# Kernel optimization log

Hardware: AMD Instinct MI355X
Metric: run time of the kernel (lower is better)

The kernel has to match this reference:

```python
import jax, jax.numpy as jnp
import numpy as np


def _pos_enc(seq_len, d_model, dtype):
    # PositionalEncoding2D buffer: interleaved sin/cos, standard transformer PE
    pos = jnp.arange(seq_len, dtype=dtype)[:, None]                      # [S,1]
    div = jnp.exp(jnp.arange(0, d_model, 2, dtype=dtype) * (-(np.log(10000.0) / d_model)))  # [d/2]
    pe = jnp.zeros((seq_len, d_model), dtype=dtype)
    pe = pe.at[:, 0::2].set(jnp.sin(pos * div))
    pe = pe.at[:, 1::2].set(jnp.cos(pos * div))
    return pe


def setup_inputs() -> dict:
    key = jax.random.key(0)
    k1, k2 = jax.random.split(key)
    B, C, H, W = 32, 384, 32, 32
    d = C
    x = jax.random.normal(k1, (B, C, H, W), dtype=jnp.float32)
    # fused QKV projection weight (stored as [d, 3d] so y = x @ W + b)
    Wqkv = jax.random.normal(k2, (d, 3 * d), dtype=jnp.float32) * (1.0 / np.sqrt(d))
    b = jnp.zeros((3 * d,), dtype=jnp.float32)
    return {"x": x, "W": Wqkv, "b": b}


def reference(x, W, b):
    B, C, H, Wd = x.shape
    d = C
    S = H * Wd
    xs = x.reshape(B, C, S).transpose(0, 2, 1)          # [B,S,d]
    xs = xs + _pos_enc(S, d, xs.dtype)                  # add positional encoding
    qkv = xs @ W + b                                    # [B,S,3d]
    q, k, v = jnp.split(qkv, 3, axis=-1)                # each [B,S,d]
    scores = jnp.einsum('bqd,bkd->bqk', q, k) / (d ** 0.5)  # [B,S,S]
    attn = jax.nn.softmax(scores, axis=-1)
    weighted = jnp.einsum('bqk,bkd->bqd', attn, v)      # [B,S,d]
    return weighted.transpose(0, 2, 1).reshape(B, C, H, Wd)
```

## Files before the change

kernel.cpp:

```cpp
#include <hip/hip_runtime.h>
#include <hip/hip_bf16.h>
#include <math.h>

typedef __attribute__((ext_vector_type(8))) __bf16 bf16x8;
typedef __attribute__((ext_vector_type(4))) float f32x4;

#define S_LEN 1024
#define D_MODEL 384
#define BATCH 32
#define N3 1152
#define KVB 32
#define NT (S_LEN / KVB)

#define MFMA16(a, b, c) __builtin_amdgcn_mfma_f32_16x16x32_bf16((a), (b), (c), 0, 0, 0)

static __device__ __forceinline__ ushort f2bf(float f) {
    __bf16 h = (__bf16)f;
    return __builtin_bit_cast(ushort, h);
}
static __device__ __forceinline__ uint pk2(float a, float b) {
    return (uint)f2bf(a) | ((uint)f2bf(b) << 16);
}

__global__ void pe_kernel(float* peT) {
    int idx = blockIdx.x * 256 + threadIdx.x;
    int k = idx >> 10, s = idx & 1023;
    float e = -(float)((k >> 1) * 2) * (logf(10000.0f) / (float)D_MODEL);
    float div = expf(e);
    float a = (float)s * div;
    peT[idx] = (k & 1) ? cosf(a) : sinf(a);
}

__global__ void wt_kernel(const float* __restrict__ W, ushort* __restrict__ Wt) {
    __shared__ float tile[32][33];
    int n0 = blockIdx.x * 32, k0 = blockIdx.y * 32;
    int tx = threadIdx.x, ty = threadIdx.y;
#pragma unroll
    for (int r = 0; r < 4; ++r) {
        int kl = ty * 4 + r;
        tile[kl][tx] = W[(size_t)(k0 + kl) * N3 + n0 + tx];
    }
    __syncthreads();
#pragma unroll
    for (int r = 0; r < 4; ++r) {
        int nl = ty * 4 + r;
        Wt[(size_t)(n0 + nl) * D_MODEL + k0 + tx] = f2bf(tile[tx][nl]);
    }
}

__global__ void astage_kernel(const float* __restrict__ x, const float* __restrict__ peT,
                              ushort* __restrict__ A) {
    __shared__ float tile[32][33];
    int s0 = blockIdx.x * 32, k0 = blockIdx.y * 32, b = blockIdx.z;
    int tx = threadIdx.x, ty = threadIdx.y;
#pragma unroll
    for (int r = 0; r < 4; ++r) {
        int kl = ty * 4 + r;
        tile[kl][tx] = x[(size_t)(b * D_MODEL + k0 + kl) * S_LEN + s0 + tx]
                     + peT[(size_t)(k0 + kl) * S_LEN + s0 + tx];
    }
    __syncthreads();
#pragma unroll
    for (int r = 0; r < 4; ++r) {
        int sl = ty * 4 + r;
        A[(size_t)(b * S_LEN + s0 + sl) * D_MODEL + k0 + tx] = f2bf(tile[tx][sl]);
    }
}

__global__ __launch_bounds__(256) void qkv_gemm(const ushort* __restrict__ A,
                                                const ushort* __restrict__ Wt,
                                                const float* __restrict__ bias,
                                                ushort* __restrict__ Qb,
                                                ushort* __restrict__ Ktl,
                                                ushort* __restrict__ Vtl) {
    __shared__ __align__(16) ushort As[128 * 32];
    __shared__ __align__(16) ushort Bs[128 * 32];
    int id = blockIdx.x;
    int g = id / 288, loc = id % 288;
    int nt_ = loc / 32, mt_ = g * 32 + (loc % 32);
    int m0 = mt_ * 128, n0 = nt_ * 128;
    int tid = threadIdx.x;
    int wave = tid >> 6, lane = tid & 63;
    int i16 = lane & 15, gq = lane >> 4;
    int wr = wave >> 1, wc = wave & 1;
    f32x4 acc[4][4] = {};
    for (int ks = 0; ks < 12; ++ks) {
        int k0 = ks * 32;
        __syncthreads();
#pragma unroll
        for (int i = 0; i < 2; ++i) {
            int off = (wave * 2 + i) * 1024;
            int row = (off >> 6) + (lane >> 2);
            int kc = lane & 3;
            const ushort* ga = A + (size_t)(m0 + row) * D_MODEL + k0 + kc * 8;
            __builtin_amdgcn_global_load_lds(
                (const __attribute__((address_space(1))) uint32_t*)ga,
                (__attribute__((address_space(3))) uint32_t*)((char*)As + off), 16, 0, 0);
            const ushort* gb = Wt + (size_t)(n0 + row) * D_MODEL + k0 + kc * 8;
            __builtin_amdgcn_global_load_lds(
                (const __attribute__((address_space(1))) uint32_t*)gb,
                (__attribute__((address_space(3))) uint32_t*)((char*)Bs + off), 16, 0, 0);
        }
        __syncthreads();
        bf16x8 af[4], bfr[4];
#pragma unroll
        for (int mt = 0; mt < 4; ++mt) {
            int row = wr * 64 + mt * 16 + i16;
            af[mt] = *reinterpret_cast<const bf16x8*>(&As[row * 32 + gq * 8]);
        }
#pragma unroll
        for (int nt = 0; nt < 4; ++nt) {
            int row = wc * 64 + nt * 16 + i16;
            bfr[nt] = *reinterpret_cast<const bf16x8*>(&Bs[row * 32 + gq * 8]);
        }
#pragma unroll
        for (int mt = 0; mt < 4; ++mt)
#pragma unroll
            for (int nt = 0; nt < 4; ++nt)
                acc[mt][nt] = MFMA16(af[mt], bfr[nt], acc[mt][nt]);
    }
    if (n0 < D_MODEL) {
#pragma unroll
        for (int nt = 0; nt < 4; ++nt) {
            int n = n0 + wc * 64 + nt * 16 + i16;
            float bv = bias[n];
#pragma unroll
            for (int mt = 0; mt < 4; ++mt)
#pragma unroll
                for (int r = 0; r < 4; ++r) {
                    int m = m0 + wr * 64 + mt * 16 + gq * 4 + r;
                    Qb[(size_t)m * D_MODEL + n] = f2bf(acc[mt][nt][r] + bv);
                }
        }
    } else if (n0 < 2 * D_MODEL) {
        int b = m0 >> 10;
#pragma unroll
        for (int nt = 0; nt < 4; ++nt) {
            int n = n0 + wc * 64 + nt * 16 + i16;
            float bv = bias[n];
            int k2 = n - D_MODEL;
            int slotx = k2 >> 3, within = k2 & 7;
#pragma unroll
            for (int mt = 0; mt < 4; ++mt)
#pragma unroll
                for (int r = 0; r < 4; ++r) {
                    int m = m0 + wr * 64 + mt * 16 + gq * 4 + r;
                    int s = m & 1023;
                    int t = s >> 5, j = s & 31;
                    size_t idx = (size_t)(b * 32 + t) * 12288 + j * 384
                               + (((slotx ^ (j & 7)) << 3) + within);
                    Ktl[idx] = f2bf(acc[mt][nt][r] + bv);
                }
        }
    } else {
        int b = m0 >> 10;
#pragma unroll
        for (int nt = 0; nt < 4; ++nt) {
            int n = n0 + wc * 64 + nt * 16 + i16;
            float bv = bias[n];
            int c = n - 2 * D_MODEL;
            int cx = (c >> 1) & 3;
#pragma unroll
            for (int mt = 0; mt < 4; ++mt) {
                int m = m0 + wr * 64 + mt * 16 + gq * 4;
                int s = m & 1023;
                int t = s >> 5, j = s & 31;
                size_t idx = (size_t)(b * 32 + t) * 12288 + c * 32
                           + ((((j >> 3) ^ cx) << 3) + (j & 7));
                ushort4 p4;
                p4.x = f2bf(acc[mt][nt][0] + bv);
                p4.y = f2bf(acc[mt][nt][1] + bv);
                p4.z = f2bf(acc[mt][nt][2] + bv);
                p4.w = f2bf(acc[mt][nt][3] + bv);
                *reinterpret_cast<ushort4*>(&Vtl[idx]) = p4;
            }
        }
    }
}

__global__ __launch_bounds__(256, 2) void attn_kernel(const ushort* __restrict__ Qb,
                                                      const ushort* __restrict__ Ktl,
                                                      const ushort* __restrict__ Vtl,
                                                      float* __restrict__ out) {
    __shared__ __align__(16) ushort Ks[32 * 384];
    __shared__ __align__(16) ushort Vts[2][384 * 32];
    __shared__ __align__(16) ushort Pq[2][4 * 32 * 8];
    __shared__ float Ltab[2][2][2][16];
    int id = blockIdx.x;
    int xcd = id & 7, slot = (id >> 3) & 3, qt = id >> 5;
    int b = slot * 8 + xcd;
    int tid = threadIdx.x;
    int wave = tid >> 6, lane = tid & 63;
    int i16 = lane & 15, gq = lane >> 4;
    int qg = wave & 1, h = wave >> 1;
    int q0w = qt * 64 + qg * 32;

    auto stage_K = [&](int tt) {
        const ushort* pan = Ktl + (size_t)(b * 32 + tt) * 12288;
#pragma unroll
        for (int r = 0; r < 6; ++r) {
            int ii = wave * 6 + r;
            const ushort* ga = pan + ii * 512 + lane * 8;
            __builtin_amdgcn_global_load_lds(
                (const __attribute__((address_space(1))) uint32_t*)ga,
                (__attribute__((address_space(3))) uint32_t*)((char*)Ks + ii * 1024), 16, 0, 0);
        }
    };
    auto stage_V = [&](int tt, int bi) {
        const ushort* pan = Vtl + (size_t)(b * 32 + tt) * 12288;
#pragma unroll
        for (int r = 0; r < 6; ++r) {
            int ii = wave * 6 + r;
            const ushort* ga = pan + ii * 512 + lane * 8;
            __builtin_amdgcn_global_load_lds(
                (const __attribute__((address_space(1))) uint32_t*)ga,
                (__attribute__((address_space(3))) uint32_t*)((char*)&Vts[bi][0] + ii * 1024), 16, 0, 0);
        }
    };

    stage_K(0);
    stage_V(0, 0);

    bf16x8 qf[12][2];
    const ushort* Qb0 = Qb + (size_t)(b * S_LEN + q0w + i16) * D_MODEL;
    const ushort* Qb1 = Qb + (size_t)(b * S_LEN + q0w + 16 + i16) * D_MODEL;
#pragma unroll
    for (int kt = 0; kt < 12; ++kt) {
        qf[kt][0] = *reinterpret_cast<const bf16x8*>(Qb0 + kt * 32 + gq * 8);
        qf[kt][1] = *reinterpret_cast<const bf16x8*>(Qb1 + kt * 32 + gq * 8);
    }

    f32x4 oc[12][2] = {};
    float lsum0 = 0.f, lsum1 = 0.f;
    const float sl2e = 0.05103103630798287f * 1.4426950408889634f;

    char* PqB = (char*)&Pq[qg][0];
    const int krow = (h * 16 + i16) * 768;
    const int ksw  = (i16 & 7) << 4;
    const int kgq  = gq * 16;
    const int vx   = (gq * 16) ^ (((i16 >> 1) & 3) << 4);

    for (int t = 0; t < NT; ++t) {
        asm volatile("s_waitcnt vmcnt(6) lgkmcnt(0)" ::: "memory");
        __builtin_amdgcn_s_barrier();
        __builtin_amdgcn_sched_barrier(0);

        const char* Kb = (const char*)Ks;
        f32x4 sacc0 = {}, sacc1 = {};
        __builtin_amdgcn_s_setprio(1);
#pragma unroll
        for (int kt = 0; kt < 12; ++kt) {
            bf16x8 kf = *reinterpret_cast<const bf16x8*>(
                Kb + krow + (((kt * 64) | kgq) ^ ksw));
            sacc0 = MFMA16(kf, qf[kt][0], sacc0);
            sacc1 = MFMA16(kf, qf[kt][1], sacc1);
        }
        __builtin_amdgcn_s_setprio(0);

        float p00 = exp2f(sacc0[0] * sl2e), p01 = exp2f(sacc0[1] * sl2e);
        float p02 = exp2f(sacc0[2] * sl2e), p03 = exp2f(sacc0[3] * sl2e);
        float p10 = exp2f(sacc1[0] * sl2e), p11 = exp2f(sacc1[1] * sl2e);
        float p12 = exp2f(sacc1[2] * sl2e), p13 = exp2f(sacc1[3] * sl2e);
        lsum0 += (p00 + p01) + (p02 + p03);
        lsum1 += (p10 + p11) + (p12 + p13);
        {
            int pw = (h * 2 + (gq >> 1)) * 512 + (gq & 1) * 8;
            uint2 w0; w0.x = pk2(p00, p01); w0.y = pk2(p02, p03);
            uint2 w1; w1.x = pk2(p10, p11); w1.y = pk2(p12, p13);
            *reinterpret_cast<uint2*>(PqB + pw + i16 * 16) = w0;
            *reinterpret_cast<uint2*>(PqB + pw + (16 + i16) * 16) = w1;
        }
        asm volatile("s_waitcnt vmcnt(0) lgkmcnt(0)" ::: "memory");
        __builtin_amdgcn_s_barrier();
        __builtin_amdgcn_sched_barrier(0);
        if (t + 1 < NT) {
            stage_K(t + 1);
            stage_V(t + 1, (t + 1) & 1);
        }

        bf16x8 pf0 = *reinterpret_cast<const bf16x8*>(PqB + gq * 512 + i16 * 16);
        bf16x8 pf1 = *reinterpret_cast<const bf16x8*>(PqB + gq * 512 + (16 + i16) * 16);
        const char* Vb = (const char*)&Vts[t & 1][0];
        __builtin_amdgcn_s_setprio(1);
#pragma unroll
        for (int ct = 0; ct < 12; ++ct) {
            bf16x8 vf = *reinterpret_cast<const bf16x8*>(
                Vb + (h * 12 + ct) * 1024 + i16 * 64 + vx);
            oc[ct][0] = MFMA16(vf, pf0, oc[ct][0]);
            oc[ct][1] = MFMA16(vf, pf1, oc[ct][1]);
        }
        __builtin_amdgcn_s_setprio(0);
    }

    lsum0 += __shfl_xor(lsum0, 16); lsum0 += __shfl_xor(lsum0, 32);
    lsum1 += __shfl_xor(lsum1, 16); lsum1 += __shfl_xor(lsum1, 32);
    __syncthreads();
    if (gq == 0) {
        Ltab[qg][h][0][i16] = lsum0;
        Ltab[qg][h][1][i16] = lsum1;
    }
    __syncthreads();
    float inv0 = 1.0f / (Ltab[qg][0][0][i16] + Ltab[qg][1][0][i16]);
    float inv1 = 1.0f / (Ltab[qg][0][1][i16] + Ltab[qg][1][1][i16]);

    float* obase = out + (size_t)b * D_MODEL * S_LEN + q0w + i16;
#pragma unroll
    for (int ct = 0; ct < 12; ++ct)
#pragma unroll
        for (int r = 0; r < 4; ++r) {
            int c = h * 192 + ct * 16 + gq * 4 + r;
            obase[(size_t)c * S_LEN] = oc[ct][0][r] * inv0;
            obase[(size_t)c * S_LEN + 16] = oc[ct][1][r] * inv1;
        }
}

extern "C" void kernel_launch(void* const* d_in, const int* in_sizes, int n_in,
                              void* d_out, int out_size, void* d_ws, size_t ws_size,
                              hipStream_t stream) {
    const float* x    = (const float*)d_in[0];
    const float* W    = (const float*)d_in[1];
    const float* bias = (const float*)d_in[2];
    float* out = (float*)d_out;

    char* ws = (char*)d_ws;
    ushort* A_bf = (ushort*)(ws);
    ushort* Wt   = (ushort*)(ws + 25165824);
    float*  peT  = (float*)(ws + 26050560);
    ushort* Qb   = (ushort*)(ws + 27623424);
    ushort* Ktl  = (ushort*)(ws + 52789248);
    ushort* Vtl  = (ushort*)(ws + 77955072);

    pe_kernel<<<1536, 256, 0, stream>>>(peT);
    wt_kernel<<<dim3(36, 12), dim3(32, 8), 0, stream>>>(W, Wt);
    astage_kernel<<<dim3(32, 12, 32), dim3(32, 8), 0, stream>>>(x, peT, A_bf);
    qkv_gemm<<<2304, 256, 0, stream>>>(A_bf, Wt, bias, Qb, Ktl, Vtl);
    attn_kernel<<<512, 256, 0, stream>>>(Qb, Ktl, Vtl, out);
}
```

Measured before the change: 155.0 us.

## Widen attention KV tile to 64 with 8 waves splitting keys and shuffled P

Doubles the key/value block per iteration to 64 and moves to 512-thread blocks where 4 query groups of 16 rows and 2 key halves share the staged K/V tiles, with a final cross-wave reduction of partial outputs through LDS. The P matrix is redistributed via lane shuffles instead of an LDS round trip, and exp and bf16 packing use raw v_exp_f32 and v_cvt_pk_bf16_f32 instructions. The QKV GEMM epilogue is changed to write the new 64-row swizzled K/V layout. The aim is fewer barriers per key and less LDS traffic, but LDS use grows to about 148 KB per block, which may limit occupancy. The wait now drains all loads before each iteration, which removes the previous overlap of prefetch with compute.

After: 161.1 us. +4.0%, slower.

```diff
diff --git a/kernel.cpp b/kernel.cpp
--- a/kernel.cpp
+++ b/kernel.cpp
@@ -9,7 +9,7 @@
 #define D_MODEL 384
 #define BATCH 32
 #define N3 1152
-#define KVB 32
+#define KVB 64
 #define NT (S_LEN / KVB)
 
 #define MFMA16(a, b, c) __builtin_amdgcn_mfma_f32_16x16x32_bf16((a), (b), (c), 0, 0, 0)
@@ -18,8 +18,11 @@
     __bf16 h = (__bf16)f;
     return __builtin_bit_cast(ushort, h);
 }
-static __device__ __forceinline__ uint pk2(float a, float b) {
-    return (uint)f2bf(a) | ((uint)f2bf(b) << 16);
+static __device__ __forceinline__ float exp2a(float x) {
+    float r; asm("v_exp_f32 %0, %1" : "=v"(r) : "v"(x)); return r;
+}
+static __device__ __forceinline__ uint cvtpk(float a, float b) {
+    uint r; asm("v_cvt_pk_bf16_f32 %0, %1, %2" : "=v"(r) : "v"(a), "v"(b)); return r;
 }
 
 __global__ void pe_kernel(float* peT) {
@@ -139,16 +142,16 @@
             int n = n0 + wc * 64 + nt * 16 + i16;
             float bv = bias[n];
             int k2 = n - D_MODEL;
-            int slotx = k2 >> 3, within = k2 & 7;
+            int slotk = k2 >> 3, within = k2 & 7;
 #pragma unroll
             for (int mt = 0; mt < 4; ++mt)
 #pragma unroll
                 for (int r = 0; r < 4; ++r) {
                     int m = m0 + wr * 64 + mt * 16 + gq * 4 + r;
                     int s = m & 1023;
-                    int t = s >> 5, j = s & 31;
-                    size_t idx = (size_t)(b * 32 + t) * 12288 + j * 384
-                               + (((slotx ^ (j & 7)) << 3) + within);
+                    int t = s >> 6, j = s & 63;
+                    size_t idx = (size_t)(b * 16 + t) * 24576 + j * 384
+                               + (((slotk ^ (j & 7)) << 3) + within);
                     Ktl[idx] = f2bf(acc[mt][nt][r] + bv);
                 }
         }
@@ -159,13 +162,13 @@
             int n = n0 + wc * 64 + nt * 16 + i16;
             float bv = bias[n];
             int c = n - 2 * D_MODEL;
-            int cx = (c >> 1) & 3;
+            int cx = c & 7;
 #pragma unroll
             for (int mt = 0; mt < 4; ++mt) {
                 int m = m0 + wr * 64 + mt * 16 + gq * 4;
                 int s = m & 1023;
-                int t = s >> 5, j = s & 31;
-                size_t idx = (size_t)(b * 32 + t) * 12288 + c * 32
+                int t = s >> 6, j = s & 63;
+                size_t idx = (size_t)(b * 16 + t) * 24576 + c * 64
                            + ((((j >> 3) ^ cx) << 3) + (j & 7));
                 ushort4 p4;
                 p4.x = f2bf(acc[mt][nt][0] + bv);
@@ -178,99 +181,101 @@
     }
 }
 
-__global__ __launch_bounds__(256, 2) void attn_kernel(const ushort* __restrict__ Qb,
+__global__ __launch_bounds__(512, 2) void attn_kernel(const ushort* __restrict__ Qb,
                                                       const ushort* __restrict__ Ktl,
                                                       const ushort* __restrict__ Vtl,
                                                       float* __restrict__ out) {
-    __shared__ __align__(16) ushort Ks[32 * 384];
-    __shared__ __align__(16) ushort Vts[2][384 * 32];
-    __shared__ __align__(16) ushort Pq[2][4 * 32 * 8];
-    __shared__ float Ltab[2][2][2][16];
+    __shared__ __align__(16) char smem[49152 * 3 + 512];
     int id = blockIdx.x;
     int xcd = id & 7, slot = (id >> 3) & 3, qt = id >> 5;
     int b = slot * 8 + xcd;
     int tid = threadIdx.x;
     int wave = tid >> 6, lane = tid & 63;
     int i16 = lane & 15, gq = lane >> 4;
-    int qg = wave & 1, h = wave >> 1;
-    int q0w = qt * 64 + qg * 32;
+    int qg = wave & 3, h = wave >> 2;
+    int q0w = qt * 64 + qg * 16;
 
     auto stage_K = [&](int tt) {
-        const ushort* pan = Ktl + (size_t)(b * 32 + tt) * 12288;
+        const ushort* pan = Ktl + (size_t)(b * 16 + tt) * 24576;
 #pragma unroll
         for (int r = 0; r < 6; ++r) {
             int ii = wave * 6 + r;
             const ushort* ga = pan + ii * 512 + lane * 8;
             __builtin_amdgcn_global_load_lds(
                 (const __attribute__((address_space(1))) uint32_t*)ga,
-                (__attribute__((address_space(3))) uint32_t*)((char*)Ks + ii * 1024), 16, 0, 0);
+                (__attribute__((address_space(3))) uint32_t*)(smem + ii * 1024), 16, 0, 0);
         }
     };
     auto stage_V = [&](int tt, int bi) {
-        const ushort* pan = Vtl + (size_t)(b * 32 + tt) * 12288;
+        const ushort* pan = Vtl + (size_t)(b * 16 + tt) * 24576;
+        char* dst = smem + 49152 + bi * 49152;
 #pragma unroll
         for (int r = 0; r < 6; ++r) {
             int ii = wave * 6 + r;
             const ushort* ga = pan + ii * 512 + lane * 8;
             __builtin_amdgcn_global_load_lds(
                 (const __attribute__((address_space(1))) uint32_t*)ga,
-                (__attribute__((address_space(3))) uint32_t*)((char*)&Vts[bi][0] + ii * 1024), 16, 0, 0);
+                (__attribute__((address_space(3))) uint32_t*)(dst + ii * 1024), 16, 0, 0);
         }
     };
 
     stage_K(0);
     stage_V(0, 0);
 
-    bf16x8 qf[12][2];
-    const ushort* Qb0 = Qb + (size_t)(b * S_LEN + q0w + i16) * D_MODEL;
-    const ushort* Qb1 = Qb + (size_t)(b * S_LEN + q0w + 16 + i16) * D_MODEL;
-#pragma unroll
-    for (int kt = 0; kt < 12; ++kt) {
-        qf[kt][0] = *reinterpret_cast<const bf16x8*>(Qb0 + kt * 32 + gq * 8);
-        qf[kt][1] = *reinterpret_cast<const bf16x8*>(Qb1 + kt * 32 + gq * 8);
-    }
-
-    f32x4 oc[12][2] = {};
-    float lsum0 = 0.f, lsum1 = 0.f;
+    bf16x8 qf[12];
+    const ushort* Qr = Qb + (size_t)(b * S_LEN + q0w + i16) * D_MODEL;
+#pragma unroll
+    for (int kt = 0; kt < 12; ++kt)
+        qf[kt] = *reinterpret_cast<const bf16x8*>(Qr + kt * 32 + gq * 8);
+
+    f32x4 oc[24] = {};
+    float lsum = 0.f;
     const float sl2e = 0.05103103630798287f * 1.4426950408889634f;
-
-    char* PqB = (char*)&Pq[qg][0];
-    const int krow = (h * 16 + i16) * 768;
-    const int ksw  = (i16 & 7) << 4;
-    const int kgq  = gq * 16;
-    const int vx   = (gq * 16) ^ (((i16 >> 1) & 3) << 4);
+    const int sw = i16 & 7;
+    const int jb = h * 32;
+    const int srcA = ((gq & 1) << 5) + i16;
+    const int srcB = srcA + 16;
+    const int jhsel = gq >> 1;
 
     for (int t = 0; t < NT; ++t) {
-        asm volatile("s_waitcnt vmcnt(6) lgkmcnt(0)" ::: "memory");
+        asm volatile("s_waitcnt vmcnt(0) lgkmcnt(0)" ::: "memory");
         __builtin_amdgcn_s_barrier();
         __builtin_amdgcn_sched_barrier(0);
 
-        const char* Kb = (const char*)Ks;
+        const char* Kb = (const char*)smem;
         f32x4 sacc0 = {}, sacc1 = {};
         __builtin_amdgcn_s_setprio(1);
 #pragma unroll
         for (int kt = 0; kt < 12; ++kt) {
-            bf16x8 kf = *reinterpret_cast<const bf16x8*>(
-                Kb + krow + (((kt * 64) | kgq) ^ ksw));
-            sacc0 = MFMA16(kf, qf[kt][0], sacc0);
-            sacc1 = MFMA16(kf, qf[kt][1], sacc1);
+            const char* k0p = Kb + (jb + i16) * 768 + (((kt * 4 + gq) ^ sw) << 4);
+            const char* k1p = Kb + (jb + 16 + i16) * 768 + (((kt * 4 + gq) ^ sw) << 4);
+            bf16x8 kf0 = *reinterpret_cast<const bf16x8*>(k0p);
+            bf16x8 kf1 = *reinterpret_cast<const bf16x8*>(k1p);
+            sacc0 = MFMA16(kf0, qf[kt], sacc0);
+            sacc1 = MFMA16(kf1, qf[kt], sacc1);
         }
         __builtin_amdgcn_s_setprio(0);
 
-        float p00 = exp2f(sacc0[0] * sl2e), p01 = exp2f(sacc0[1] * sl2e);
-        float p02 = exp2f(sacc0[2] * sl2e), p03 = exp2f(sacc0[3] * sl2e);
-        float p10 = exp2f(sacc1[0] * sl2e), p11 = exp2f(sacc1[1] * sl2e);
-        float p12 = exp2f(sacc1[2] * sl2e), p13 = exp2f(sacc1[3] * sl2e);
-        lsum0 += (p00 + p01) + (p02 + p03);
-        lsum1 += (p10 + p11) + (p12 + p13);
-        {
-            int pw = (h * 2 + (gq >> 1)) * 512 + (gq & 1) * 8;
-            uint2 w0; w0.x = pk2(p00, p01); w0.y = pk2(p02, p03);
-            uint2 w1; w1.x = pk2(p10, p11); w1.y = pk2(p12, p13);
-            *reinterpret_cast<uint2*>(PqB + pw + i16 * 16) = w0;
-            *reinterpret_cast<uint2*>(PqB + pw + (16 + i16) * 16) = w1;
-        }
-        asm volatile("s_waitcnt vmcnt(0) lgkmcnt(0)" ::: "memory");
+        float p00 = exp2a(sacc0[0] * sl2e), p01 = exp2a(sacc0[1] * sl2e);
+        float p02 = exp2a(sacc0[2] * sl2e), p03 = exp2a(sacc0[3] * sl2e);
+        float p10 = exp2a(sacc1[0] * sl2e), p11 = exp2a(sacc1[1] * sl2e);
+        float p12 = exp2a(sacc1[2] * sl2e), p13 = exp2a(sacc1[3] * sl2e);
+        lsum += ((p00 + p01) + (p02 + p03)) + ((p10 + p11) + (p12 + p13));
+
+        uint u00 = cvtpk(p00, p01), u01 = cvtpk(p02, p03);
+        uint u10 = cvtpk(p10, p11), u11 = cvtpk(p12, p13);
+        uint tA0 = __shfl(u00, srcA, 64), tA1 = __shfl(u10, srcA, 64);
+        uint tA2 = __shfl(u01, srcA, 64), tA3 = __shfl(u11, srcA, 64);
+        uint tB0 = __shfl(u00, srcB, 64), tB1 = __shfl(u10, srcB, 64);
+        uint tB2 = __shfl(u01, srcB, 64), tB3 = __shfl(u11, srcB, 64);
+        uint4 wv;
+        wv.x = jhsel ? tA1 : tA0;
+        wv.y = jhsel ? tA3 : tA2;
+        wv.z = jhsel ? tB1 : tB0;
+        wv.w = jhsel ? tB3 : tB2;
+        bf16x8 pf = __builtin_bit_cast(bf16x8, wv);
+
+        asm volatile("s_waitcnt lgkmcnt(0)" ::: "memory");
         __builtin_amdgcn_s_barrier();
         __builtin_amdgcn_sched_barrier(0);
         if (t + 1 < NT) {
@@ -278,40 +283,44 @@
             stage_V(t + 1, (t + 1) & 1);
         }
 
-        bf16x8 pf0 = *reinterpret_cast<const bf16x8*>(PqB + gq * 512 + i16 * 16);
-        bf16x8 pf1 = *reinterpret_cast<const bf16x8*>(PqB + gq * 512 + (16 + i16) * 16);
-        const char* Vb = (const char*)&Vts[t & 1][0];
+        const char* Vb = smem + 49152 + (t & 1) * 49152;
         __builtin_amdgcn_s_setprio(1);
 #pragma unroll
-        for (int ct = 0; ct < 12; ++ct) {
-            bf16x8 vf = *reinterpret_cast<const bf16x8*>(
-                Vb + (h * 12 + ct) * 1024 + i16 * 64 + vx);
-            oc[ct][0] = MFMA16(vf, pf0, oc[ct][0]);
-            oc[ct][1] = MFMA16(vf, pf1, oc[ct][1]);
+        for (int ct = 0; ct < 24; ++ct) {
+            const char* vp = Vb + (ct * 16 + i16) * 128 + (((h * 4 + gq) ^ sw) << 4);
+            bf16x8 vf = *reinterpret_cast<const bf16x8*>(vp);
+            oc[ct] = MFMA16(vf, pf, oc[ct]);
         }
         __builtin_amdgcn_s_setprio(0);
     }
 
-    lsum0 += __shfl_xor(lsum0, 16); lsum0 += __shfl_xor(lsum0, 32);
-    lsum1 += __shfl_xor(lsum1, 16); lsum1 += __shfl_xor(lsum1, 32);
+    lsum += __shfl_xor(lsum, 16);
+    lsum += __shfl_xor(lsum, 32);
     __syncthreads();
-    if (gq == 0) {
-        Ltab[qg][h][0][i16] = lsum0;
-        Ltab[qg][h][1][i16] = lsum1;
+    float* Ored = (float*)smem;
+    float* Lred = (float*)(smem + 98304);
+    if (h == 0) {
+        float* Oq = Ored + qg * 6144;
+#pragma unroll
+        for (int ct = 0; ct < 24; ++ct)
+#pragma unroll
+            for (int r = 0; r < 4; ++r)
+                Oq[(ct * 16 + gq * 4 + r) * 16 + i16] = oc[ct][r];
+        if (gq == 0) Lred[qg * 16 + i16] = lsum;
     }
     __syncthreads();
-    float inv0 = 1.0f / (Ltab[qg][0][0][i16] + Ltab[qg][1][0][i16]);
-    float inv1 = 1.0f / (Ltab[qg][0][1][i16] + Ltab[qg][1][1][i16]);
-
-    float* obase = out + (size_t)b * D_MODEL * S_LEN + q0w + i16;
-#pragma unroll
-    for (int ct = 0; ct < 12; ++ct)
-#pragma unroll
-        for (int r = 0; r < 4; ++r) {
-            int c = h * 192 + ct * 16 + gq * 4 + r;
-            obase[(size_t)c * S_LEN] = oc[ct][0][r] * inv0;
-            obase[(size_t)c * S_LEN + 16] = oc[ct][1][r] * inv1;
-        }
+    if (h == 1) {
+        const float* Oq = Ored + qg * 6144;
+        float inv = 1.0f / (lsum + Lred[qg * 16 + i16]);
+        float* ob = out + (size_t)b * D_MODEL * S_LEN + q0w + i16;
+#pragma unroll
+        for (int ct = 0; ct < 24; ++ct)
+#pragma unroll
+            for (int r = 0; r < 4; ++r) {
+                int c = ct * 16 + gq * 4 + r;
+                ob[(size_t)c * S_LEN] = (oc[ct][r] + Oq[c * 16 + i16]) * inv;
+            }
+    }
 }
 
 extern "C" void kernel_launch(void* const* d_in, const int* in_sizes, int n_in,
@@ -334,5 +343,5 @@
     wt_kernel<<<dim3(36, 12), dim3(32, 8), 0, stream>>>(W, Wt);
     astage_kernel<<<dim3(32, 12, 32), dim3(32, 8), 0, stream>>>(x, peT, A_bf);
     qkv_gemm<<<2304, 256, 0, stream>>>(A_bf, Wt, bias, Qb, Ktl, Vtl);
-    attn_kernel<<<512, 256, 0, stream>>>(Qb, Ktl, Vtl, out);
-}
+    attn_kernel<<<512, 512, 0, stream>>>(Qb, Ktl, Vtl, out);
+}
```

## Warp-specialize attention into QK/softmax and PV waves with 128-query blocks

Applied to the files above, without the earlier changes.

Rewrites the attention kernel into a 512-thread block covering 128 queries. Four waves compute QK^T and exp and write P to double-buffered LDS, while four other waves run PV one tile behind, with K and V each double-buffered and software-pipelined. The goal is to overlap the softmax/QK phase with the PV MFMAs and to halve K/V re-staging per query. Exp and bf16 packing are swapped for raw v_exp_f32 and v_cvt_pk_bf16_f32 instructions. This raises LDS use and register pressure (48 accumulators per PV wave) and halves the grid to 256 blocks, which may leave some CUs idle.

Result: faster. 139.1 us (-10.3%).

```diff
diff --git a/kernel.cpp b/kernel.cpp
--- a/kernel.cpp
+++ b/kernel.cpp
@@ -18,8 +18,11 @@
     __bf16 h = (__bf16)f;
     return __builtin_bit_cast(ushort, h);
 }
-static __device__ __forceinline__ uint pk2(float a, float b) {
-    return (uint)f2bf(a) | ((uint)f2bf(b) << 16);
+static __device__ __forceinline__ float exp2a(float x) {
+    float r; asm("v_exp_f32 %0, %1" : "=v"(r) : "v"(x)); return r;
+}
+static __device__ __forceinline__ uint cvtpk(float a, float b) {
+    uint r; asm("v_cvt_pk_bf16_f32 %0, %1, %2" : "=v"(r) : "v"(a), "v"(b)); return r;
 }
 
 __global__ void pe_kernel(float* peT) {
@@ -139,7 +142,7 @@
             int n = n0 + wc * 64 + nt * 16 + i16;
             float bv = bias[n];
             int k2 = n - D_MODEL;
-            int slotx = k2 >> 3, within = k2 & 7;
+            int slotk = k2 >> 3, within = k2 & 7;
 #pragma unroll
             for (int mt = 0; mt < 4; ++mt)
 #pragma unroll
@@ -148,7 +151,7 @@
                     int s = m & 1023;
                     int t = s >> 5, j = s & 31;
                     size_t idx = (size_t)(b * 32 + t) * 12288 + j * 384
-                               + (((slotx ^ (j & 7)) << 3) + within);
+                               + (((slotk ^ (j & 7)) << 3) + within);
                     Ktl[idx] = f2bf(acc[mt][nt][r] + bv);
                 }
         }
@@ -178,140 +181,187 @@
     }
 }
 
-__global__ __launch_bounds__(256, 2) void attn_kernel(const ushort* __restrict__ Qb,
+__global__ __launch_bounds__(512, 1) void attn_kernel(const ushort* __restrict__ Qb,
                                                       const ushort* __restrict__ Ktl,
                                                       const ushort* __restrict__ Vtl,
                                                       float* __restrict__ out) {
-    __shared__ __align__(16) ushort Ks[32 * 384];
-    __shared__ __align__(16) ushort Vts[2][384 * 32];
-    __shared__ __align__(16) ushort Pq[2][4 * 32 * 8];
-    __shared__ float Ltab[2][2][2][16];
+    __shared__ __align__(16) char smem[114688];
     int id = blockIdx.x;
     int xcd = id & 7, slot = (id >> 3) & 3, qt = id >> 5;
     int b = slot * 8 + xcd;
+    int q0blk = qt * 128;
     int tid = threadIdx.x;
     int wave = tid >> 6, lane = tid & 63;
     int i16 = lane & 15, gq = lane >> 4;
-    int qg = wave & 1, h = wave >> 1;
-    int q0w = qt * 64 + qg * 32;
-
-    auto stage_K = [&](int tt) {
+    int w2 = wave & 3;
+    const float sl2e = 0.05103103630798287f * 1.4426950408889634f;
+
+    auto stage_K = [&](int tt, int bi) {
         const ushort* pan = Ktl + (size_t)(b * 32 + tt) * 12288;
-#pragma unroll
-        for (int r = 0; r < 6; ++r) {
-            int ii = wave * 6 + r;
+        char* dst = smem + bi * 24576;
+#pragma unroll
+        for (int r = 0; r < 3; ++r) {
+            int ii = wave * 3 + r;
             const ushort* ga = pan + ii * 512 + lane * 8;
             __builtin_amdgcn_global_load_lds(
                 (const __attribute__((address_space(1))) uint32_t*)ga,
-                (__attribute__((address_space(3))) uint32_t*)((char*)Ks + ii * 1024), 16, 0, 0);
+                (__attribute__((address_space(3))) uint32_t*)(dst + ii * 1024), 16, 0, 0);
         }
     };
     auto stage_V = [&](int tt, int bi) {
         const ushort* pan = Vtl + (size_t)(b * 32 + tt) * 12288;
-#pragma unroll
-        for (int r = 0; r < 6; ++r) {
-            int ii = wave * 6 + r;
+        char* dst = smem + 49152 + bi * 24576;
+#pragma unroll
+        for (int r = 0; r < 3; ++r) {
+            int ii = wave * 3 + r;
             const ushort* ga = pan + ii * 512 + lane * 8;
             __builtin_amdgcn_global_load_lds(
                 (const __attribute__((address_space(1))) uint32_t*)ga,
-                (__attribute__((address_space(3))) uint32_t*)((char*)&Vts[bi][0] + ii * 1024), 16, 0, 0);
+                (__attribute__((address_space(3))) uint32_t*)(dst + ii * 1024), 16, 0, 0);
         }
     };
 
-    stage_K(0);
-    stage_V(0, 0);
-
-    bf16x8 qf[12][2];
-    const ushort* Qb0 = Qb + (size_t)(b * S_LEN + q0w + i16) * D_MODEL;
-    const ushort* Qb1 = Qb + (size_t)(b * S_LEN + q0w + 16 + i16) * D_MODEL;
-#pragma unroll
-    for (int kt = 0; kt < 12; ++kt) {
-        qf[kt][0] = *reinterpret_cast<const bf16x8*>(Qb0 + kt * 32 + gq * 8);
-        qf[kt][1] = *reinterpret_cast<const bf16x8*>(Qb1 + kt * 32 + gq * 8);
-    }
-
-    f32x4 oc[12][2] = {};
-    float lsum0 = 0.f, lsum1 = 0.f;
-    const float sl2e = 0.05103103630798287f * 1.4426950408889634f;
-
-    char* PqB = (char*)&Pq[qg][0];
-    const int krow = (h * 16 + i16) * 768;
-    const int ksw  = (i16 & 7) << 4;
-    const int kgq  = gq * 16;
-    const int vx   = (gq * 16) ^ (((i16 >> 1) & 3) << 4);
-
-    for (int t = 0; t < NT; ++t) {
-        asm volatile("s_waitcnt vmcnt(6) lgkmcnt(0)" ::: "memory");
+    stage_K(0, 0);
+    asm volatile("s_waitcnt vmcnt(0)" ::: "memory");
+    __syncthreads();
+
+    if (wave < 4) {
+        int qg = w2;
+        bf16x8 qf[12][2];
+        const ushort* Q0 = Qb + (size_t)(b * S_LEN + q0blk + qg * 32 + i16) * D_MODEL;
+        const ushort* Q1 = Q0 + (size_t)16 * D_MODEL;
+#pragma unroll
+        for (int kt = 0; kt < 12; ++kt) {
+            qf[kt][0] = *reinterpret_cast<const bf16x8*>(Q0 + kt * 32 + gq * 8);
+            qf[kt][1] = *reinterpret_cast<const bf16x8*>(Q1 + kt * 32 + gq * 8);
+        }
+        float lsum0 = 0.f, lsum1 = 0.f;
+        int jc0 = gq >> 1, jc1 = 2 + (gq >> 1);
+        int q0 = qg * 32 + i16, q1 = qg * 32 + 16 + i16;
+
+        auto qk_step = [&](int tt) {
+            const char* Kb = smem + (tt & 1) * 24576;
+            char* Pw = smem + 98304 + (tt & 1) * 8192;
+            f32x4 s00 = {}, s01 = {}, s10 = {}, s11 = {};
+            __builtin_amdgcn_s_setprio(1);
+#pragma unroll
+            for (int kt = 0; kt < 12; ++kt) {
+                int kc = (kt * 64 + gq * 16) ^ ((i16 & 7) << 4);
+                bf16x8 kf0 = *reinterpret_cast<const bf16x8*>(Kb + i16 * 768 + kc);
+                bf16x8 kf1 = *reinterpret_cast<const bf16x8*>(Kb + (16 + i16) * 768 + kc);
+                s00 = MFMA16(kf0, qf[kt][0], s00);
+                s01 = MFMA16(kf0, qf[kt][1], s01);
+                s10 = MFMA16(kf1, qf[kt][0], s10);
+                s11 = MFMA16(kf1, qf[kt][1], s11);
+            }
+            __builtin_amdgcn_s_setprio(0);
+            {
+                float p0 = exp2a(s00[0] * sl2e), p1 = exp2a(s00[1] * sl2e);
+                float p2 = exp2a(s00[2] * sl2e), p3 = exp2a(s00[3] * sl2e);
+                lsum0 += (p0 + p1) + (p2 + p3);
+                uint2 w; w.x = cvtpk(p0, p1); w.y = cvtpk(p2, p3);
+                *reinterpret_cast<uint2*>(Pw + jc0 * 2048 + ((q0 * 16) ^ ((jc0 & 3) << 4)) + (gq & 1) * 8) = w;
+            }
+            {
+                float p0 = exp2a(s01[0] * sl2e), p1 = exp2a(s01[1] * sl2e);
+                float p2 = exp2a(s01[2] * sl2e), p3 = exp2a(s01[3] * sl2e);
+                lsum1 += (p0 + p1) + (p2 + p3);
+                uint2 w; w.x = cvtpk(p0, p1); w.y = cvtpk(p2, p3);
+                *reinterpret_cast<uint2*>(Pw + jc0 * 2048 + ((q1 * 16) ^ ((jc0 & 3) << 4)) + (gq & 1) * 8) = w;
+            }
+            {
+                float p0 = exp2a(s10[0] * sl2e), p1 = exp2a(s10[1] * sl2e);
+                float p2 = exp2a(s10[2] * sl2e), p3 = exp2a(s10[3] * sl2e);
+                lsum0 += (p0 + p1) + (p2 + p3);
+                uint2 w; w.x = cvtpk(p0, p1); w.y = cvtpk(p2, p3);
+                *reinterpret_cast<uint2*>(Pw + jc1 * 2048 + ((q0 * 16) ^ ((jc1 & 3) << 4)) + (gq & 1) * 8) = w;
+            }
+            {
+                float p0 = exp2a(s11[0] * sl2e), p1 = exp2a(s11[1] * sl2e);
+                float p2 = exp2a(s11[2] * sl2e), p3 = exp2a(s11[3] * sl2e);
+                lsum1 += (p0 + p1) + (p2 + p3);
+                uint2 w; w.x = cvtpk(p0, p1); w.y = cvtpk(p2, p3);
+                *reinterpret_cast<uint2*>(Pw + jc1 * 2048 + ((q1 * 16) ^ ((jc1 & 3) << 4)) + (gq & 1) * 8) = w;
+            }
+        };
+
+        qk_step(0);
+        stage_K(1, 1);
+        stage_V(0, 0);
+        asm volatile("s_waitcnt lgkmcnt(0)" ::: "memory");
         __builtin_amdgcn_s_barrier();
-        __builtin_amdgcn_sched_barrier(0);
-
-        const char* Kb = (const char*)Ks;
-        f32x4 sacc0 = {}, sacc1 = {};
-        __builtin_amdgcn_s_setprio(1);
-#pragma unroll
-        for (int kt = 0; kt < 12; ++kt) {
-            bf16x8 kf = *reinterpret_cast<const bf16x8*>(
-                Kb + krow + (((kt * 64) | kgq) ^ ksw));
-            sacc0 = MFMA16(kf, qf[kt][0], sacc0);
-            sacc1 = MFMA16(kf, qf[kt][1], sacc1);
-        }
-        __builtin_amdgcn_s_setprio(0);
-
-        float p00 = exp2f(sacc0[0] * sl2e), p01 = exp2f(sacc0[1] * sl2e);
-        float p02 = exp2f(sacc0[2] * sl2e), p03 = exp2f(sacc0[3] * sl2e);
-        float p10 = exp2f(sacc1[0] * sl2e), p11 = exp2f(sacc1[1] * sl2e);
-        float p12 = exp2f(sacc1[2] * sl2e), p13 = exp2f(sacc1[3] * sl2e);
-        lsum0 += (p00 + p01) + (p02 + p03);
-        lsum1 += (p10 + p11) + (p12 + p13);
-        {
-            int pw = (h * 2 + (gq >> 1)) * 512 + (gq & 1) * 8;
-            uint2 w0; w0.x = pk2(p00, p01); w0.y = pk2(p02, p03);
-            uint2 w1; w1.x = pk2(p10, p11); w1.y = pk2(p12, p13);
-            *reinterpret_cast<uint2*>(PqB + pw + i16 * 16) = w0;
-            *reinterpret_cast<uint2*>(PqB + pw + (16 + i16) * 16) = w1;
-        }
-        asm volatile("s_waitcnt vmcnt(0) lgkmcnt(0)" ::: "memory");
+        for (int t = 0; t < NT; ++t) {
+            asm volatile("s_waitcnt vmcnt(0) lgkmcnt(0)" ::: "memory");
+            __builtin_amdgcn_s_barrier();
+            __builtin_amdgcn_sched_barrier(0);
+            if (t + 2 < NT) stage_K(t + 2, t & 1);
+            if (t + 1 < NT) stage_V(t + 1, (t + 1) & 1);
+            if (t + 1 < NT) qk_step(t + 1);
+        }
+        __syncthreads();
+        lsum0 += __shfl_xor(lsum0, 16); lsum0 += __shfl_xor(lsum0, 32);
+        lsum1 += __shfl_xor(lsum1, 16); lsum1 += __shfl_xor(lsum1, 32);
+        float* Lt = reinterpret_cast<float*>(smem + 98304);
+        if (gq == 0) {
+            Lt[qg * 32 + i16] = lsum0;
+            Lt[qg * 32 + 16 + i16] = lsum1;
+        }
+        __syncthreads();
+    } else {
+        int cs = w2;
+        f32x4 oc[6][8] = {};
+        stage_K(1, 1);
+        stage_V(0, 0);
+        asm volatile("s_waitcnt lgkmcnt(0)" ::: "memory");
         __builtin_amdgcn_s_barrier();
-        __builtin_amdgcn_sched_barrier(0);
-        if (t + 1 < NT) {
-            stage_K(t + 1);
-            stage_V(t + 1, (t + 1) & 1);
-        }
-
-        bf16x8 pf0 = *reinterpret_cast<const bf16x8*>(PqB + gq * 512 + i16 * 16);
-        bf16x8 pf1 = *reinterpret_cast<const bf16x8*>(PqB + gq * 512 + (16 + i16) * 16);
-        const char* Vb = (const char*)&Vts[t & 1][0];
-        __builtin_amdgcn_s_setprio(1);
-#pragma unroll
-        for (int ct = 0; ct < 12; ++ct) {
-            bf16x8 vf = *reinterpret_cast<const bf16x8*>(
-                Vb + (h * 12 + ct) * 1024 + i16 * 64 + vx);
-            oc[ct][0] = MFMA16(vf, pf0, oc[ct][0]);
-            oc[ct][1] = MFMA16(vf, pf1, oc[ct][1]);
-        }
-        __builtin_amdgcn_s_setprio(0);
-    }
-
-    lsum0 += __shfl_xor(lsum0, 16); lsum0 += __shfl_xor(lsum0, 32);
-    lsum1 += __shfl_xor(lsum1, 16); lsum1 += __shfl_xor(lsum1, 32);
-    __syncthreads();
-    if (gq == 0) {
-        Ltab[qg][h][0][i16] = lsum0;
-        Ltab[qg][h][1][i16] = lsum1;
-    }
-    __syncthreads();
-    float inv0 = 1.0f / (Ltab[qg][0][0][i16] + Ltab[qg][1][0][i16]);
-    float inv1 = 1.0f / (Ltab[qg][0][1][i16] + Ltab[qg][1][1][i16]);
-
-    float* obase = out + (size_t)b * D_MODEL * S_LEN + q0w + i16;
-#pragma unroll
-    for (int ct = 0; ct < 12; ++ct)
-#pragma unroll
-        for (int r = 0; r < 4; ++r) {
-            int c = h * 192 + ct * 16 + gq * 4 + r;
-            obase[(size_t)c * S_LEN] = oc[ct][0][r] * inv0;
-            obase[(size_t)c * S_LEN + 16] = oc[ct][1][r] * inv1;
-        }
+        for (int t = 0; t < NT; ++t) {
+            asm volatile("s_waitcnt vmcnt(0) lgkmcnt(0)" ::: "memory");
+            __builtin_amdgcn_s_barrier();
+            __builtin_amdgcn_sched_barrier(0);
+            if (t + 2 < NT) stage_K(t + 2, t & 1);
+            if (t + 1 < NT) stage_V(t + 1, (t + 1) & 1);
+            const char* Vb = smem + 49152 + (t & 1) * 24576;
+            const char* Pb = smem + 98304 + (t & 1) * 8192;
+            bf16x8 pf[8];
+#pragma unroll
+            for (int qs = 0; qs < 8; ++qs) {
+                int q = qs * 16 + i16;
+                pf[qs] = *reinterpret_cast<const bf16x8*>(
+                    Pb + gq * 2048 + ((q * 16) ^ ((gq & 3) << 4)));
+            }
+            __builtin_amdgcn_s_setprio(1);
+#pragma unroll
+            for (int ct = 0; ct < 6; ++ct) {
+                int c = cs * 96 + ct * 16 + i16;
+                bf16x8 vf = *reinterpret_cast<const bf16x8*>(
+                    Vb + c * 64 + ((gq * 16) ^ (((i16 >> 1) & 3) << 4)));
+                oc[ct][0] = MFMA16(vf, pf[0], oc[ct][0]);
+                oc[ct][1] = MFMA16(vf, pf[1], oc[ct][1]);
+                oc[ct][2] = MFMA16(vf, pf[2], oc[ct][2]);
+                oc[ct][3] = MFMA16(vf, pf[3], oc[ct][3]);
+                oc[ct][4] = MFMA16(vf, pf[4], oc[ct][4]);
+                oc[ct][5] = MFMA16(vf, pf[5], oc[ct][5]);
+                oc[ct][6] = MFMA16(vf, pf[6], oc[ct][6]);
+                oc[ct][7] = MFMA16(vf, pf[7], oc[ct][7]);
+            }
+            __builtin_amdgcn_s_setprio(0);
+        }
+        __syncthreads();
+        __syncthreads();
+        const float* Lt = reinterpret_cast<const float*>(smem + 98304);
+        float* ob = out + (size_t)b * D_MODEL * S_LEN + q0blk;
+#pragma unroll
+        for (int qs = 0; qs < 8; ++qs) {
+            float inv = 1.0f / Lt[qs * 16 + i16];
+#pragma unroll
+            for (int ct = 0; ct < 6; ++ct)
+#pragma unroll
+                for (int r = 0; r < 4; ++r) {
+                    int c = cs * 96 + ct * 16 + gq * 4 + r;
+                    ob[(size_t)c * S_LEN + qs * 16 + i16] = oc[ct][qs][r] * inv;
+                }
+        }
+    }
 }
 
 extern "C" void kernel_launch(void* const* d_in, const int* in_sizes, int n_in,
@@ -334,5 +384,5 @@
     wt_kernel<<<dim3(36, 12), dim3(32, 8), 0, stream>>>(W, Wt);
     astage_kernel<<<dim3(32, 12, 32), dim3(32, 8), 0, stream>>>(x, peT, A_bf);
     qkv_gemm<<<2304, 256, 0, stream>>>(A_bf, Wt, bias, Qb, Ktl, Vtl);
-    attn_kernel<<<512, 256, 0, stream>>>(Qb, Ktl, Vtl, out);
-}
+    attn_kernel<<<256, 512, 0, stream>>>(Qb, Ktl, Vtl, out);
+}
```
